# Kernel tuning notes

Measured on AMD Instinct MI355X. Metric: run time of the kernel, lower is better.

## Reference

```python
import jax, jax.numpy as jnp
import numpy as np

B, S, V, E, H, A, L = 64, 256, 32000, 512, 512, 512, 2
EPS = 1e-5


def _ln(x, g, b):
    m = jnp.mean(x, axis=-1, keepdims=True)
    v = jnp.mean((x - m) ** 2, axis=-1, keepdims=True)
    return (x - m) * jax.lax.rsqrt(v + EPS) * g + b


def _lstm_cell(x, h, c, W_ih, W_hh, b_ih, b_hh):
    # torch gate order: i, f, g, o
    gates = x @ W_ih.T + b_ih + h @ W_hh.T + b_hh  # [B, 4H]
    i, f, g, o = jnp.split(gates, 4, axis=-1)
    i, f, o = jax.nn.sigmoid(i), jax.nn.sigmoid(f), jax.nn.sigmoid(o)
    g = jnp.tanh(g)
    c_new = f * c + i * g
    h_new = o * jnp.tanh(c_new)
    return h_new, c_new


def setup_inputs() -> dict:
    key = jax.random.key(0)
    ks = jax.random.split(key, 24)
    d = {}
    d['input_token'] = jax.random.randint(ks[0], (B, 1), 0, V)
    d['h0'] = jax.random.normal(ks[1], (L, B, H), jnp.float32)
    d['c0'] = jax.random.normal(ks[2], (L, B, H), jnp.float32)
    d['encoder_outputs'] = jax.random.normal(ks[3], (B, S, 2 * H), jnp.float32)
    d['encoder_mask'] = jnp.ones((B, S), jnp.int32)
    sc = lambda fi, fo: float(np.sqrt(6.0 / (fi + fo)))
    d['emb'] = jax.random.normal(ks[4], (V, E), jnp.float32) * 0.1
    d['ln_emb_g'] = jnp.ones((E,), jnp.float32)
    d['ln_emb_b'] = jnp.zeros((E,), jnp.float32)
    d['W_enc'] = jax.random.uniform(ks[5], (A, 2 * H), jnp.float32, -sc(2 * H, A), sc(2 * H, A))
    d['b_enc'] = jnp.zeros((A,), jnp.float32)
    d['W_dec'] = jax.random.uniform(ks[6], (A, H), jnp.float32, -sc(H, A), sc(H, A))
    d['b_dec'] = jnp.zeros((A,), jnp.float32)
    d['v_att'] = jax.random.uniform(ks[7], (1, A), jnp.float32, -sc(A, 1), sc(A, 1))
    d['ln_att_g'] = jnp.ones((A,), jnp.float32)
    d['ln_att_b'] = jnp.zeros((A,), jnp.float32)
    in0, in1 = E + 2 * H, H
    d['W_ih0'] = jax.random.uniform(ks[8], (4 * H, in0), jnp.float32, -sc(in0, 4 * H), sc(in0, 4 * H))
    d['W_hh0'] = jax.random.normal(ks[9], (4 * H, H), jnp.float32) * 0.05
    d['b_ih0'] = jnp.zeros((4 * H,), jnp.float32).at[H:2 * H].set(1.0)
    d['b_hh0'] = jnp.zeros((4 * H,), jnp.float32)
    d['W_ih1'] = jax.random.uniform(ks[10], (4 * H, in1), jnp.float32, -sc(in1, 4 * H), sc(in1, 4 * H))
    d['W_hh1'] = jax.random.normal(ks[11], (4 * H, H), jnp.float32) * 0.05
    d['b_ih1'] = jnp.zeros((4 * H,), jnp.float32).at[H:2 * H].set(1.0)
    d['b_hh1'] = jnp.zeros((4 * H,), jnp.float32)
    d['ln_lstm_g'] = jnp.ones((H,), jnp.float32)
    d['ln_lstm_b'] = jnp.zeros((H,), jnp.float32)
    d['W_ctx'] = jax.random.uniform(ks[12], (H, 2 * H), jnp.float32, -sc(2 * H, H), sc(2 * H, H))
    d['b_ctx'] = jnp.zeros((H,), jnp.float32)
    d['W_out'] = jax.random.uniform(ks[13], (V, H), jnp.float32, -sc(H, V), sc(H, V))
    d['b_out'] = jnp.zeros((V,), jnp.float32)
    return d


def reference(input_token, h0, c0, encoder_outputs, encoder_mask,
              emb, ln_emb_g, ln_emb_b,
              W_enc, b_enc, W_dec, b_dec, v_att, ln_att_g, ln_att_b,
              W_ih0, W_hh0, b_ih0, b_hh0, W_ih1, W_hh1, b_ih1, b_hh1,
              ln_lstm_g, ln_lstm_b, W_ctx, b_ctx, W_out, b_out):
    # embedding + norm (dropout = identity in eval)
    embedded = _ln(emb[input_token], ln_emb_g, ln_emb_b)  # [B,1,E]

    # attention using top-layer hidden state
    dec_h = h0[-1]  # [B,H]
    enc_proj = jnp.einsum('bsk,ak->bsa', encoder_outputs, W_enc) + b_enc
    dec_proj = dec_h @ W_dec.T + b_dec  # [B,A]
    combined = _ln(enc_proj + dec_proj[:, None, :], ln_att_g, ln_att_b)
    scores = jnp.einsum('bsa,a->bs', jnp.tanh(combined), v_att[0])
    scores = jnp.where(encoder_mask == 0, -jnp.inf, scores)
    attn_w = jax.nn.softmax(scores, axis=1)  # [B,S]
    context = jnp.einsum('bs,bsk->bk', attn_w, encoder_outputs)  # [B,2H]

    # single-step 2-layer LSTM
    x = jnp.concatenate([embedded[:, 0, :], context], axis=-1)  # [B,E+2H]
    h_l0, c_l0 = _lstm_cell(x, h0[0], c0[0], W_ih0, W_hh0, b_ih0, b_hh0)
    h_l1, c_l1 = _lstm_cell(h_l0, h0[1], c0[1], W_ih1, W_hh1, b_ih1, b_hh1)
    h_new = jnp.stack([h_l0, h_l1])
    c_new = jnp.stack([c_l0, c_l1])

    lstm_out = _ln(h_l1, ln_lstm_g, ln_lstm_b)  # [B,H]
    proj_ctx = context @ W_ctx.T + b_ctx  # [B,H]
    logits = (lstm_out + proj_ctx) @ W_out.T + b_out  # [B,V]
    return logits[:, None, :], (h_new, c_new), attn_w
```

## Files before the change

kernel.cpp:

```cpp
#include <hip/hip_runtime.h>

typedef unsigned int u32;
typedef unsigned short u16;
typedef __attribute__((ext_vector_type(8))) short short8;
typedef __attribute__((ext_vector_type(4))) float f32x4;

__device__ __forceinline__ float bf2f(u16 u) {
  union { u32 i; float f; } v; v.i = ((u32)u) << 16; return v.f;
}
__device__ __forceinline__ u16 f2bf(float f) {
  union { float f; u32 i; } v; v.f = f;
  u32 u = v.i;
  u += 0x7FFFu + ((u >> 16) & 1u);
  return (u16)(u >> 16);
}
__device__ __forceinline__ float tanh_fast(float x) {
  float e = __expf(-2.f * fabsf(x));
  float r = (1.f - e) / (1.f + e);
  return x < 0.f ? -r : r;
}
__device__ __forceinline__ float sigmoid_fast(float x) {
  return 1.f / (1.f + __expf(-x));
}
template<bool F32>
__device__ __forceinline__ float ld1(const void* p, size_t i) {
  return F32 ? ((const float*)p)[i] : bf2f(((const u16*)p)[i]);
}
__device__ __forceinline__ void outst(void* p, size_t i, float v, int f32o) {
  if (f32o) ((float*)p)[i] = v; else ((u16*)p)[i] = f2bf(v);
}

#define GLL16(gp, lp) __builtin_amdgcn_global_load_lds( \
    (__attribute__((address_space(1))) void*)(gp), \
    (__attribute__((address_space(3))) void*)(lp), 16, 0, 0)

#define OFF_H    2048000
#define OFF_C    2113536
#define OFF_ATTN 2179072

#define A_LNAG 0
#define A_LNAB 512
#define A_VAT  1024
#define A_BENC 1536
#define A_BDEC 2048
#define A_BIH0 2560
#define A_BHH0 4608
#define A_BIH1 6656
#define A_BHH1 8704
#define A_LNLG 10752
#define A_LNLB 11264
#define A_BCTX 11776
#define A_BOUT 12288
#define A_TOTAL 44288

struct SrcPtrs {
  const void *h0, *c0, *emb, *lneg, *lneb, *Wenc, *benc, *Wdec, *bdec, *vat,
             *lnag, *lnab, *bih0, *bhh0, *bih1, *bhh1, *lnlg, *lnlb, *Wctx,
             *bctx, *bout;
  const int *tok;
};

__global__ void k_flag(const u32* __restrict__ lneg, int* __restrict__ flag) {
  if (threadIdx.x == 0) flag[0] = (lneg[0] == 0x3F800000u) ? 1 : 0;
}

template<bool F32>
__device__ __forceinline__ void convblk(const void* src, u16* dst, size_t base) {
  size_t i0 = base + (size_t)threadIdx.x * 16;
  if (F32) {
    const float* s = (const float*)src + i0;
    float4 a = *(const float4*)s, b = *(const float4*)(s + 4);
    float4 c = *(const float4*)(s + 8), d = *(const float4*)(s + 12);
    short8 v0, v1;
    v0[0]=(short)f2bf(a.x); v0[1]=(short)f2bf(a.y); v0[2]=(short)f2bf(a.z); v0[3]=(short)f2bf(a.w);
    v0[4]=(short)f2bf(b.x); v0[5]=(short)f2bf(b.y); v0[6]=(short)f2bf(b.z); v0[7]=(short)f2bf(b.w);
    v1[0]=(short)f2bf(c.x); v1[1]=(short)f2bf(c.y); v1[2]=(short)f2bf(c.z); v1[3]=(short)f2bf(c.w);
    v1[4]=(short)f2bf(d.x); v1[5]=(short)f2bf(d.y); v1[6]=(short)f2bf(d.z); v1[7]=(short)f2bf(d.w);
    *(short8*)(dst + i0) = v0; *(short8*)(dst + i0 + 8) = v1;
  } else {
    const uint4* s = (const uint4*)((const u16*)src + i0);
    uint4 a = s[0], b = s[1];
    *(uint4*)(dst + i0) = a; *((uint4*)(dst + i0) + 1) = b;
  }
}

template<bool F32>
__global__ __launch_bounds__(256) void k_conv(
    const int* __restrict__ flagp, SrcPtrs P,
    u16* __restrict__ xcat, u16* __restrict__ xcat1, u16* __restrict__ h1bf,
    float* __restrict__ c0f, float* __restrict__ arena,
    u16* __restrict__ Wencbf, u16* __restrict__ Wdecbf, u16* __restrict__ Wctxbf)
{
  if (flagp[0] != (F32 ? 1 : 0)) return;
  __shared__ float red[8];
  const int t = threadIdx.x;
  const int blk = blockIdx.x;
  if (blk < 64) {
    const int b = blk;
    const int tk = P.tok[b];
    float e0 = ld1<F32>(P.emb, (size_t)tk * 512 + t);
    float e1 = ld1<F32>(P.emb, (size_t)tk * 512 + t + 256);
    float s = e0 + e1, ss = e0 * e0 + e1 * e1;
    #pragma unroll
    for (int o = 1; o < 64; o <<= 1) { s += __shfl_xor(s, o, 64); ss += __shfl_xor(ss, o, 64); }
    if ((t & 63) == 0) { red[t >> 6] = s; red[4 + (t >> 6)] = ss; }
    __syncthreads();
    s = red[0] + red[1] + red[2] + red[3];
    ss = red[4] + red[5] + red[6] + red[7];
    const float mean = s * (1.f / 512.f);
    const float rstd = rsqrtf(fmaxf(ss * (1.f / 512.f) - mean * mean, 0.f) + 1e-5f);
    xcat[b*2048 + t]       = f2bf((e0 - mean) * rstd * ld1<F32>(P.lneg, t) + ld1<F32>(P.lneb, t));
    xcat[b*2048 + t + 256] = f2bf((e1 - mean) * rstd * ld1<F32>(P.lneg, t + 256) + ld1<F32>(P.lneb, t + 256));
    xcat[b*2048 + 1536 + t]       = f2bf(ld1<F32>(P.h0, (size_t)b * 512 + t));
    xcat[b*2048 + 1536 + t + 256] = f2bf(ld1<F32>(P.h0, (size_t)b * 512 + t + 256));
  } else if (blk < 128) {
    const int b = blk - 64;
    for (int j = t; j < 512; j += 256) {
      float h1 = ld1<F32>(P.h0, 32768 + (size_t)b * 512 + j);
      xcat1[b*1024 + 512 + j] = f2bf(h1);
      h1bf[b*512 + j] = f2bf(h1);
      c0f[b*512 + j]         = ld1<F32>(P.c0, (size_t)b * 512 + j);
      c0f[32768 + b*512 + j] = ld1<F32>(P.c0, 32768 + (size_t)b * 512 + j);
    }
  } else if (blk < 256) {
    const int qb = (blk - 128) * 512;
    #pragma unroll
    for (int u = 0; u < 2; u++) {
      int Qi = qb + u * 256 + t;
      int kc = Qi >> 11, rem = Qi & 2047;
      int cq = rem >> 9, col = rem & 511;
      size_t src = (size_t)col * 1024 + kc * 32 + cq * 8;
      if (F32) {
        const float* s = (const float*)P.Wenc + src;
        float4 a = *(const float4*)s, b2 = *(const float4*)(s + 4);
        short8 v;
        v[0]=(short)f2bf(a.x); v[1]=(short)f2bf(a.y); v[2]=(short)f2bf(a.z); v[3]=(short)f2bf(a.w);
        v[4]=(short)f2bf(b2.x); v[5]=(short)f2bf(b2.y); v[6]=(short)f2bf(b2.z); v[7]=(short)f2bf(b2.w);
        *(short8*)(Wencbf + (size_t)Qi * 8) = v;
      } else {
        *(uint4*)(Wencbf + (size_t)Qi * 8) = *(const uint4*)((const u16*)P.Wenc + src);
      }
    }
  } else if (blk < 320) {
    convblk<F32>(P.Wdec, Wdecbf, (size_t)(blk - 256) * 4096);
  } else if (blk < 448) {
    convblk<F32>(P.Wctx, Wctxbf, (size_t)(blk - 320) * 4096);
  } else {
    int base = (blk - 448) * 4096;
    for (int i = t; i < 4096; i += 256) {
      int v = base + i;
      if (v >= A_TOTAL) break;
      const void* s; int off;
      if      (v < 512)   { s = P.lnag; off = v; }
      else if (v < 1024)  { s = P.lnab; off = v - 512; }
      else if (v < 1536)  { s = P.vat;  off = v - 1024; }
      else if (v < 2048)  { s = P.benc; off = v - 1536; }
      else if (v < 2560)  { s = P.bdec; off = v - 2048; }
      else if (v < 4608)  { s = P.bih0; off = v - 2560; }
      else if (v < 6656)  { s = P.bhh0; off = v - 4608; }
      else if (v < 8704)  { s = P.bih1; off = v - 6656; }
      else if (v < 10752) { s = P.bhh1; off = v - 8704; }
      else if (v < 11264) { s = P.lnlg; off = v - 10752; }
      else if (v < 11776) { s = P.lnlb; off = v - 11264; }
      else if (v < 12288) { s = P.bctx; off = v - 11776; }
      else                { s = P.bout; off = v - 12288; }
      arena[v] = ld1<F32>(s, off);
    }
  }
}

__global__ __launch_bounds__(256) void k_dproj(
    const u16* __restrict__ h1bf, const u16* __restrict__ Wdecbf,
    const float* __restrict__ arena, float* __restrict__ dpf)
{
  __shared__ float hs[512];
  __shared__ float part[256];
  const int t = threadIdx.x;
  const int b = blockIdx.x >> 2, cg = blockIdx.x & 3;
  {
    u32 u2 = *(const u32*)(h1bf + b * 512 + t * 2);
    hs[t * 2]     = bf2f((u16)(u2 & 0xffff));
    hs[t * 2 + 1] = bf2f((u16)(u2 >> 16));
  }
  __syncthreads();
  const int col = cg * 128 + (t & 127);
  const int kh = (t >> 7) * 256;
  const u16* w = Wdecbf + (size_t)col * 512 + kh;
  float acc = 0.f;
  #pragma unroll 4
  for (int k = 0; k < 256; k += 8) {
    short8 wv = *(const short8*)(w + k);
    #pragma unroll
    for (int i = 0; i < 8; i++) acc += hs[kh + k + i] * bf2f((u16)wv[i]);
  }
  part[t] = acc;
  __syncthreads();
  if (t < 128) {
    float v = part[t] + part[t + 128];
    dpf[b * 512 + col] = v + arena[A_BENC + col] + arena[A_BDEC + col];
  }
}

__global__ __launch_bounds__(512, 2) void k_scores(
    const int* __restrict__ flagp,
    const void* __restrict__ enc, const u16* __restrict__ WencT,
    const float* __restrict__ dpf, const float* __restrict__ arena,
    const int* __restrict__ mask, float* __restrict__ scores)
{
  const int f32w = flagp[0];
  __shared__ __align__(16) char sm[73728];
  const int t = threadIdx.x, wave = t >> 6, lane = t & 63;
  const int q = lane >> 4, r15 = lane & 15;
  const int m0 = blockIdx.x * 64, b = m0 >> 8, n0 = wave * 64;
  const int arow = t >> 2, acq = t & 3;

  float4 rA0, rA1;

  auto stageB = [&](int buf, int kt) {
    char* Bb = sm + buf * 32768;
    #pragma unroll
    for (int r = 0; r < 4; ++r) {
      int chunk = (wave << 2) + r;
      const u16* g = WencT + (size_t)kt * 16384 + (size_t)(chunk * 64 + lane) * 8;
      GLL16(g, Bb + chunk * 1024);
    }
  };
  auto stageAb = [&](int buf, int kc) {
    if (wave < 4) {
      int row = lane ^ (wave << 1);
      const u16* g = (const u16*)enc + (size_t)(m0 + row) * 1024 + kc + (wave << 3);
      GLL16(g, sm + 65536 + buf * 4096 + (wave << 10));
    }
  };
  auto issueAf = [&](int kc) {
    const float* p = (const float*)enc + (size_t)(m0 + arow) * 1024 + kc + (acq << 3);
    rA0 = *(const float4*)p; rA1 = *(const float4*)(p + 4);
  };
  auto writeAf = [&](int buf) {
    short8 v;
    v[0]=(short)f2bf(rA0.x); v[1]=(short)f2bf(rA0.y); v[2]=(short)f2bf(rA0.z); v[3]=(short)f2bf(rA0.w);
    v[4]=(short)f2bf(rA1.x); v[5]=(short)f2bf(rA1.y); v[6]=(short)f2bf(rA1.z); v[7]=(short)f2bf(rA1.w);
    int slot = (acq << 6) + (arow ^ (acq << 1));
    *(short8*)(sm + 65536 + buf * 4096 + slot * 16) = v;
  };

  if (f32w) { if (t < 256) issueAf(0); }
  stageB(0, 0);
  if (!f32w) stageAb(0, 0);
  if (f32w && t < 256) writeAf(0);
  __syncthreads();

  f32x4 acc[4][4] = {};
  int cur = 0;
  for (int kt = 0; kt < 32; ++kt) {
    const int more = (kt + 1 < 32);
    if (more) {
      if (f32w) { if (t < 256) issueAf((kt + 1) << 5); }
      stageB(cur ^ 1, kt + 1);
      if (!f32w) stageAb(cur ^ 1, (kt + 1) << 5);
    }
    const char* Ab = sm + 65536 + cur * 4096;
    const char* Bb = sm + cur * 32768;
    short8 af[4], bfr[4];
    #pragma unroll
    for (int mi = 0; mi < 4; mi++) {
      int slot = (q << 6) + ((mi * 16 + r15) ^ (q << 1));
      af[mi] = *(const short8*)(Ab + slot * 16);
    }
    #pragma unroll
    for (int ni = 0; ni < 4; ni++)
      bfr[ni] = *(const short8*)(Bb + ((q << 9) + n0 + ni * 16 + r15) * 16);
    #pragma unroll
    for (int mi = 0; mi < 4; mi++)
      #pragma unroll
      for (int ni = 0; ni < 4; ni++)
        acc[mi][ni] = __builtin_amdgcn_mfma_f32_16x16x32_bf16(af[mi], bfr[ni], acc[mi][ni], 0, 0, 0);
    if (more && f32w && t < 256) writeAf(cur ^ 1);
    __syncthreads();
    cur ^= 1;
  }

  float dpv[4];
  #pragma unroll
  for (int ni = 0; ni < 4; ni++)
    dpv[ni] = dpf[b * 512 + n0 + ni * 16 + r15];

  float* ps    = (float*)sm;
  float* pq    = (float*)(sm + 2048);
  float* mean_ = (float*)(sm + 4096);
  float* rstd_ = (float*)(sm + 4352);
  #pragma unroll
  for (int mi = 0; mi < 4; mi++)
    #pragma unroll
    for (int r = 0; r < 4; r++) {
      float s = 0.f, sq = 0.f;
      #pragma unroll
      for (int ni = 0; ni < 4; ni++) {
        float x = acc[mi][ni][r] + dpv[ni];
        s += x; sq += x * x;
      }
      #pragma unroll
      for (int o = 1; o < 16; o <<= 1) { s += __shfl_xor(s, o, 64); sq += __shfl_xor(sq, o, 64); }
      if (r15 == 0) { int row = mi*16 + q*4 + r; ps[wave*64 + row] = s; pq[wave*64 + row] = sq; }
    }
  __syncthreads();
  if (t < 64) {
    float s = 0.f, sq = 0.f;
    #pragma unroll
    for (int w = 0; w < 8; w++) { s += ps[w*64 + t]; sq += pq[w*64 + t]; }
    float mn = s * (1.f / 512.f);
    mean_[t] = mn;
    rstd_[t] = rsqrtf(fmaxf(sq * (1.f / 512.f) - mn * mn, 0.f) + 1e-5f);
  }
  __syncthreads();
  float g4[4], b4[4], v4[4];
  #pragma unroll
  for (int ni = 0; ni < 4; ni++) {
    int col = n0 + ni*16 + r15;
    g4[ni] = arena[A_LNAG + col]; b4[ni] = arena[A_LNAB + col]; v4[ni] = arena[A_VAT + col];
  }
  #pragma unroll
  for (int mi = 0; mi < 4; mi++)
    #pragma unroll
    for (int r = 0; r < 4; r++) {
      int row = mi*16 + q*4 + r;
      float mn = mean_[row], rs = rstd_[row];
      float s = 0.f;
      #pragma unroll
      for (int ni = 0; ni < 4; ni++) {
        float x = acc[mi][ni][r] + dpv[ni];
        float y = (x - mn) * rs * g4[ni] + b4[ni];
        s += tanh_fast(y) * v4[ni];
      }
      #pragma unroll
      for (int o = 1; o < 16; o <<= 1) s += __shfl_xor(s, o, 64);
      if (r15 == 0) ps[wave*64 + row] = s;
    }
  __syncthreads();
  if (t < 64) {
    float sc = 0.f;
    #pragma unroll
    for (int w = 0; w < 8; w++) sc += ps[w*64 + t];
    int s_ = (m0 & 255) + t;
    scores[m0 + t] = mask[b*256 + s_] ? sc : -__builtin_inff();
  }
}

__global__ __launch_bounds__(256) void k_softmax_ctx(
    const int* __restrict__ flagp,
    const float* __restrict__ scores, const void* __restrict__ enc,
    u16* __restrict__ xcat, void* __restrict__ out)
{
  const int f32w = flagp[0];
  __shared__ float aw[256];
  __shared__ float red[8];
  __shared__ float px[512];
  const int t = threadIdx.x;
  const int b = blockIdx.x >> 2, kq = blockIdx.x & 3;
  float sv = scores[b * 256 + t];
  float mx = sv;
  #pragma unroll
  for (int o = 1; o < 64; o <<= 1) mx = fmaxf(mx, __shfl_xor(mx, o, 64));
  if ((t & 63) == 0) red[t >> 6] = mx;
  __syncthreads();
  mx = fmaxf(fmaxf(red[0], red[1]), fmaxf(red[2], red[3]));
  float e = __expf(sv - mx);
  float s = e;
  #pragma unroll
  for (int o = 1; o < 64; o <<= 1) s += __shfl_xor(s, o, 64);
  if ((t & 63) == 0) red[4 + (t >> 6)] = s;
  __syncthreads();
  s = red[4] + red[5] + red[6] + red[7];
  float w = e / s;
  aw[t] = w;
  if (kq == 0) outst(out, OFF_ATTN + b * 256 + t, w, f32w);
  __syncthreads();
  const int kk = t & 127, sg = t >> 7;
  float a0 = 0.f, a1 = 0.f;
  if (f32w) {
    const float* p = (const float*)enc + (size_t)b * 262144 + kq * 256 + kk * 2;
    #pragma unroll 4
    for (int i = 0; i < 128; i++) {
      int si = i * 2 + sg;
      float2 v = *(const float2*)(p + (size_t)si * 1024);
      a0 += aw[si] * v.x; a1 += aw[si] * v.y;
    }
  } else {
    const u16* p = (const u16*)enc + (size_t)b * 262144 + kq * 256 + kk * 2;
    #pragma unroll 4
    for (int i = 0; i < 128; i++) {
      int si = i * 2 + sg;
      u32 u = *(const u32*)(p + (size_t)si * 1024);
      a0 += aw[si] * bf2f((u16)(u & 0xffff)); a1 += aw[si] * bf2f((u16)(u >> 16));
    }
  }
  px[sg * 256 + kk * 2]     = a0;
  px[sg * 256 + kk * 2 + 1] = a1;
  __syncthreads();
  float cv = px[t] + px[256 + t];
  xcat[b * 2048 + 512 + kq * 256 + t] = f2bf(cv);
}

__global__ __launch_bounds__(512) void k_lstm(
    const int* __restrict__ flagp,
    const u16* __restrict__ x, int K,
    const void* __restrict__ Wa, int Ka,
    const void* __restrict__ Wb, int Kb,
    int boff_ih, int boff_hh,
    const float* __restrict__ arena, const float* __restrict__ c0f, int coff,
    void* __restrict__ out, size_t h_off, size_t c_off,
    u16* __restrict__ aux_bf, float* __restrict__ aux_f)
{
  const int f32w = flagp[0];
  __shared__ __align__(16) char sm[40960];
  const int t = threadIdx.x, wave = t >> 6, lane = t & 63;
  const int q = lane >> 4, r15 = lane & 15;
  const int jt = blockIdx.x;
  const int kslice = K >> 3, ksteps = kslice >> 5;
  const int k0 = wave * kslice;
  const void* W; int Kw, koff;
  if (k0 < Ka) { W = Wa; Kw = Ka; koff = k0; }
  else         { W = Wb; Kw = Kb; koff = k0 - Ka; }
  char* slab = sm + wave * 5120;
  const int bc = lane >> 2, bcq = lane & 3;
  const int wrow = (bc >> 2) * 512 + jt * 4 + (bc & 3);
  f32x4 acc4[4] = {};

  for (int st = 0; st < ksteps; ++st) {
    const int kA = k0 + st * 32;
    const int kB = koff + st * 32;
    #pragma unroll
    for (int i = 0; i < 4; i++) {
      int id = i * 64 + lane;
      int row = id >> 2, cq = id & 3;
      *(uint4*)(slab + (cq * 64 + row) * 16) = *(const uint4*)(x + (size_t)row * K + kA + cq * 8);
    }
    {
      size_t wi = (size_t)wrow * Kw + kB + bcq * 8;
      short8 bv;
      if (f32w) {
        const float* wp = (const float*)W + wi;
        float4 a = *(const float4*)wp, b = *(const float4*)(wp + 4);
        bv[0]=(short)f2bf(a.x); bv[1]=(short)f2bf(a.y); bv[2]=(short)f2bf(a.z); bv[3]=(short)f2bf(a.w);
        bv[4]=(short)f2bf(b.x); bv[5]=(short)f2bf(b.y); bv[6]=(short)f2bf(b.z); bv[7]=(short)f2bf(b.w);
      } else {
        bv = *(const short8*)((const u16*)W + wi);
      }
      *(short8*)(slab + 4096 + (bcq * 16 + bc) * 16) = bv;
    }
    short8 af[4];
    #pragma unroll
    for (int mi = 0; mi < 4; mi++)
      af[mi] = *(const short8*)(slab + (q * 64 + mi * 16 + r15) * 16);
    short8 bfrg = *(const short8*)(slab + 4096 + (q * 16 + r15) * 16);
    #pragma unroll
    for (int mi = 0; mi < 4; mi++)
      acc4[mi] = __builtin_amdgcn_mfma_f32_16x16x32_bf16(af[mi], bfrg, acc4[mi], 0, 0, 0);
  }
  __syncthreads();
  float* part = (float*)sm;
  #pragma unroll
  for (int mi = 0; mi < 4; mi++)
    #pragma unroll
    for (int r = 0; r < 4; r++)
      part[wave * 1024 + (mi * 16 + q * 4 + r) * 16 + r15] = acc4[mi][r];
  __syncthreads();
  if (t < 256) {
    const int b_ = t >> 2, cl = t & 3;
    const int jg = jt * 4 + cl;
    float g4[4];
    #pragma unroll
    for (int g = 0; g < 4; g++) {
      float v = 0.f;
      #pragma unroll
      for (int w = 0; w < 8; w++) v += part[w * 1024 + b_ * 16 + g * 4 + cl];
      g4[g] = v + arena[boff_ih + g * 512 + jg] + arena[boff_hh + g * 512 + jg];
    }
    float i_ = sigmoid_fast(g4[0]), f_ = sigmoid_fast(g4[1]), o_ = sigmoid_fast(g4[3]);
    float gg = tanh_fast(g4[2]);
    float c_ = f_ * c0f[coff + b_ * 512 + jg] + i_ * gg;
    float h_ = o_ * tanh_fast(c_);
    outst(out, h_off + b_ * 512 + jg, h_, f32w);
    outst(out, c_off + b_ * 512 + jg, c_, f32w);
    if (aux_bf) aux_bf[b_ * 1024 + jg] = f2bf(h_);
    if (aux_f)  aux_f[b_ * 512 + jg] = h_;
  }
}

__global__ __launch_bounds__(256) void k_svec(
    const float* __restrict__ hl1f, const u16* __restrict__ xcat,
    const u16* __restrict__ Wctxbf, const float* __restrict__ arena,
    u16* __restrict__ svec)
{
  __shared__ float ctx[1024];
  __shared__ float red[8];
  const int t = threadIdx.x, b = blockIdx.x;
  for (int i = t; i < 1024; i += 256) ctx[i] = bf2f(xcat[b * 2048 + 512 + i]);
  float h0v = hl1f[b * 512 + t], h1v = hl1f[b * 512 + t + 256];
  float s = h0v + h1v, ss = h0v * h0v + h1v * h1v;
  #pragma unroll
  for (int o = 1; o < 64; o <<= 1) { s += __shfl_xor(s, o, 64); ss += __shfl_xor(ss, o, 64); }
  if ((t & 63) == 0) { red[t >> 6] = s; red[4 + (t >> 6)] = ss; }
  __syncthreads();
  s = red[0] + red[1] + red[2] + red[3];
  ss = red[4] + red[5] + red[6] + red[7];
  const float mean = s * (1.f / 512.f);
  const float rstd = rsqrtf(fmaxf(ss * (1.f / 512.f) - mean * mean, 0.f) + 1e-5f);
  for (int hh = t; hh < 512; hh += 256) {
    float hv = hl1f[b * 512 + hh];
    float lnv = (hv - mean) * rstd * arena[A_LNLG + hh] + arena[A_LNLB + hh];
    float acc = arena[A_BCTX + hh];
    #pragma unroll 4
    for (int k = 0; k < 1024; k += 8) {
      short8 wv = *(const short8*)(Wctxbf + (size_t)hh * 1024 + k);
      #pragma unroll
      for (int i = 0; i < 8; i++) acc += ctx[k + i] * bf2f((u16)wv[i]);
    }
    svec[b * 512 + hh] = f2bf(lnv + acc);
  }
}

__global__ __launch_bounds__(256) void k_logits(
    const int* __restrict__ flagp,
    const u16* __restrict__ svec, const void* __restrict__ Wout,
    const float* __restrict__ arena, void* __restrict__ out)
{
  const int f32w = flagp[0];
  __shared__ __align__(16) char sm[8192];
  const int t = threadIdx.x, wave = t >> 6, lane = t & 63;
  const int q = lane >> 4, r15 = lane & 15;
  const int nb = blockIdx.x * 128;
  float4 ra[2], rb[2]; uint4 rc[2];
  auto issue = [&](int kc) {
    #pragma unroll
    for (int i = 0; i < 2; i++) {
      int c = i * 256 + t;
      int row = c >> 2, cq = c & 3;
      size_t off = (size_t)(nb + row) * 512 + kc * 32 + cq * 8;
      if (f32w) {
        const float* p = (const float*)Wout + off;
        ra[i] = *(const float4*)p; rb[i] = *(const float4*)(p + 4);
      } else {
        rc[i] = *(const uint4*)((const u16*)Wout + off);
      }
    }
  };
  issue(0);
  f32x4 acc[4][2] = {};
  for (int kc = 0; kc < 16; kc++) {
    #pragma unroll
    for (int i = 0; i < 2; i++) {
      int c = i * 256 + t;
      int row = c >> 2, cq = c & 3;
      if (f32w) {
        short8 v;
        v[0]=(short)f2bf(ra[i].x); v[1]=(short)f2bf(ra[i].y); v[2]=(short)f2bf(ra[i].z); v[3]=(short)f2bf(ra[i].w);
        v[4]=(short)f2bf(rb[i].x); v[5]=(short)f2bf(rb[i].y); v[6]=(short)f2bf(rb[i].z); v[7]=(short)f2bf(rb[i].w);
        *(short8*)(sm + (cq * 128 + row) * 16) = v;
      } else {
        *(uint4*)(sm + (cq * 128 + row) * 16) = rc[i];
      }
    }
    __syncthreads();
    if (kc + 1 < 16) issue(kc + 1);
    short8 af[4], bfr[2];
    #pragma unroll
    for (int mi = 0; mi < 4; mi++)
      af[mi] = *(const short8*)(svec + (size_t)(mi * 16 + r15) * 512 + kc * 32 + q * 8);
    #pragma unroll
    for (int ni = 0; ni < 2; ni++)
      bfr[ni] = *(const short8*)(sm + (q * 128 + wave * 32 + ni * 16 + r15) * 16);
    #pragma unroll
    for (int mi = 0; mi < 4; mi++)
      #pragma unroll
      for (int ni = 0; ni < 2; ni++)
        acc[mi][ni] = __builtin_amdgcn_mfma_f32_16x16x32_bf16(af[mi], bfr[ni], acc[mi][ni], 0, 0, 0);
    __syncthreads();
  }
  #pragma unroll
  for (int ni = 0; ni < 2; ni++) {
    int col = nb + wave * 32 + ni * 16 + r15;
    float bo = arena[A_BOUT + col];
    #pragma unroll
    for (int mi = 0; mi < 4; mi++)
      #pragma unroll
      for (int r = 0; r < 4; r++) {
        int brow = mi * 16 + q * 4 + r;
        outst(out, (size_t)brow * 32000 + col, acc[mi][ni][r] + bo, f32w);
      }
  }
}

extern "C" void kernel_launch(void* const* d_in, const int* in_sizes, int n_in,
                              void* d_out, int out_size, void* d_ws, size_t ws_size,
                              hipStream_t stream)
{
  SrcPtrs P;
  P.tok  = (const int*)d_in[0];
  P.h0   = d_in[1];  P.c0   = d_in[2];
  const void* enc = d_in[3];
  const int* mask = (const int*)d_in[4];
  P.emb  = d_in[5]; P.lneg = d_in[6]; P.lneb = d_in[7];
  P.Wenc = d_in[8]; P.benc = d_in[9]; P.Wdec = d_in[10]; P.bdec = d_in[11];
  P.vat  = d_in[12]; P.lnag = d_in[13]; P.lnab = d_in[14];
  P.bih0 = d_in[17]; P.bhh0 = d_in[18];
  P.bih1 = d_in[21]; P.bhh1 = d_in[22];
  P.lnlg = d_in[23]; P.lnlb = d_in[24];
  P.Wctx = d_in[25]; P.bctx = d_in[26];
  const void* Wout = d_in[27];
  P.bout = d_in[28];
  const void* Wih0 = d_in[15];
  const void* Whh0 = d_in[16];
  const void* Wih1 = d_in[19];
  const void* Whh1 = d_in[20];

  char* ws = (char*)d_ws;
  int*   flag    = (int*)(ws + 0);
  float* arena   = (float*)(ws + 256);
  u16*   Wencbf  = (u16*)(ws + 177664);
  u16*   Wdecbf  = (u16*)(ws + 1226240);
  u16*   Wctxbf  = (u16*)(ws + 1750528);
  u16*   xcat    = (u16*)(ws + 2799104);
  u16*   xcat1   = (u16*)(ws + 3061248);
  u16*   h1bf    = (u16*)(ws + 3192320);
  float* c0f     = (float*)(ws + 3257856);
  float* scores  = (float*)(ws + 3520000);
  float* hl1f    = (float*)(ws + 3585536);
  u16*   svec    = (u16*)(ws + 3716608);
  float* dpf     = (float*)(ws + 3782144);

  k_flag<<<1, 64, 0, stream>>>((const u32*)P.lneg, flag);
  k_conv<false><<<460, 256, 0, stream>>>(flag, P, xcat, xcat1, h1bf, c0f, arena, Wencbf, Wdecbf, Wctxbf);
  k_conv<true ><<<460, 256, 0, stream>>>(flag, P, xcat, xcat1, h1bf, c0f, arena, Wencbf, Wdecbf, Wctxbf);
  k_dproj<<<256, 256, 0, stream>>>(h1bf, Wdecbf, arena, dpf);
  k_scores<<<256, 512, 0, stream>>>(flag, enc, Wencbf, dpf, arena, mask, scores);
  k_softmax_ctx<<<256, 256, 0, stream>>>(flag, scores, enc, xcat, d_out);
  k_lstm<<<128, 512, 0, stream>>>(flag, xcat, 2048, Wih0, 1536, Whh0, 512,
                                  A_BIH0, A_BHH0, arena, c0f, 0,
                                  d_out, OFF_H, OFF_C, xcat1, (float*)nullptr);
  k_lstm<<<128, 512, 0, stream>>>(flag, xcat1, 1024, Wih1, 512, Whh1, 512,
                                  A_BIH1, A_BHH1, arena, c0f, 32768,
                                  d_out, OFF_H + 32768, OFF_C + 32768,
                                  (u16*)nullptr, hl1f);
  k_svec<<<64, 256, 0, stream>>>(hl1f, xcat, Wctxbf, arena, svec);
  k_logits<<<250, 256, 0, stream>>>(flag, svec, Wout, arena, d_out);
}
```

Baseline: 388.2 us.

## Halve M-tile in scores and N-tile in logits, widen context loads, double-buffer logits

The scores kernel now processes 32 encoder rows per block instead of 64 and launches 512 blocks, with the A-tile staging and the LN reductions resized to match. The logits kernel uses 64 output columns per block across 500 blocks and gains a double-buffered LDS pipeline, so the next K-chunk's global loads overlap the MFMAs. The softmax-context kernel reads four values per thread with float4 loads over four s-groups. The aim is more blocks across the many CUs and better latency hiding in the memory-bound stages. The cost is less reuse of the staged W_enc tile per block, since each block still loads the full B operand for only half as many rows.

```diff
diff --git a/kernel.cpp b/kernel.cpp
--- a/kernel.cpp
+++ b/kernel.cpp
@@ -201,17 +201,17 @@
   }
 }
 
-__global__ __launch_bounds__(512, 2) void k_scores(
+__global__ __launch_bounds__(512, 4) void k_scores(
     const int* __restrict__ flagp,
     const void* __restrict__ enc, const u16* __restrict__ WencT,
     const float* __restrict__ dpf, const float* __restrict__ arena,
     const int* __restrict__ mask, float* __restrict__ scores)
 {
   const int f32w = flagp[0];
-  __shared__ __align__(16) char sm[73728];
+  __shared__ __align__(16) char sm[69632];
   const int t = threadIdx.x, wave = t >> 6, lane = t & 63;
   const int q = lane >> 4, r15 = lane & 15;
-  const int m0 = blockIdx.x * 64, b = m0 >> 8, n0 = wave * 64;
+  const int m0 = blockIdx.x * 32, b = m0 >> 8, n0 = wave * 64;
   const int arow = t >> 2, acq = t & 3;
 
   float4 rA0, rA1;
@@ -226,10 +226,12 @@
     }
   };
   auto stageAb = [&](int buf, int kc) {
-    if (wave < 4) {
-      int row = lane ^ (wave << 1);
-      const u16* g = (const u16*)enc + (size_t)(m0 + row) * 1024 + kc + (wave << 3);
-      GLL16(g, sm + 65536 + buf * 4096 + (wave << 10));
+    if (wave < 2) {
+      int s = (wave << 6) + lane;
+      int cq = s >> 5, rowslot = s & 31;
+      int row = rowslot ^ (cq << 1);
+      const u16* g = (const u16*)enc + (size_t)(m0 + row) * 1024 + kc + (cq << 3);
+      GLL16(g, sm + 65536 + buf * 2048 + (wave << 10));
     }
   };
   auto issueAf = [&](int kc) {
@@ -240,42 +242,42 @@
     short8 v;
     v[0]=(short)f2bf(rA0.x); v[1]=(short)f2bf(rA0.y); v[2]=(short)f2bf(rA0.z); v[3]=(short)f2bf(rA0.w);
     v[4]=(short)f2bf(rA1.x); v[5]=(short)f2bf(rA1.y); v[6]=(short)f2bf(rA1.z); v[7]=(short)f2bf(rA1.w);
-    int slot = (acq << 6) + (arow ^ (acq << 1));
-    *(short8*)(sm + 65536 + buf * 4096 + slot * 16) = v;
+    int slot = (acq << 5) + (arow ^ (acq << 1));
+    *(short8*)(sm + 65536 + buf * 2048 + slot * 16) = v;
   };
 
-  if (f32w) { if (t < 256) issueAf(0); }
+  if (f32w) { if (t < 128) issueAf(0); }
   stageB(0, 0);
   if (!f32w) stageAb(0, 0);
-  if (f32w && t < 256) writeAf(0);
-  __syncthreads();
-
-  f32x4 acc[4][4] = {};
+  if (f32w && t < 128) writeAf(0);
+  __syncthreads();
+
+  f32x4 acc[2][4] = {};
   int cur = 0;
   for (int kt = 0; kt < 32; ++kt) {
     const int more = (kt + 1 < 32);
     if (more) {
-      if (f32w) { if (t < 256) issueAf((kt + 1) << 5); }
+      if (f32w) { if (t < 128) issueAf((kt + 1) << 5); }
       stageB(cur ^ 1, kt + 1);
       if (!f32w) stageAb(cur ^ 1, (kt + 1) << 5);
     }
-    const char* Ab = sm + 65536 + cur * 4096;
+    const char* Ab = sm + 65536 + cur * 2048;
     const char* Bb = sm + cur * 32768;
-    short8 af[4], bfr[4];
-    #pragma unroll
-    for (int mi = 0; mi < 4; mi++) {
-      int slot = (q << 6) + ((mi * 16 + r15) ^ (q << 1));
+    short8 af[2], bfr[4];
+    #pragma unroll
+    for (int mi = 0; mi < 2; mi++) {
+      int slot = (q << 5) + ((mi * 16 + r15) ^ (q << 1));
       af[mi] = *(const short8*)(Ab + slot * 16);
     }
     #pragma unroll
     for (int ni = 0; ni < 4; ni++)
       bfr[ni] = *(const short8*)(Bb + ((q << 9) + n0 + ni * 16 + r15) * 16);
     #pragma unroll
-    for (int mi = 0; mi < 4; mi++)
+    for (int mi = 0; mi < 2; mi++)
       #pragma unroll
       for (int ni = 0; ni < 4; ni++)
         acc[mi][ni] = __builtin_amdgcn_mfma_f32_16x16x32_bf16(af[mi], bfr[ni], acc[mi][ni], 0, 0, 0);
-    if (more && f32w && t < 256) writeAf(cur ^ 1);
+    if (more && f32w && t < 128) writeAf(cur ^ 1);
     __syncthreads();
     cur ^= 1;
   }
@@ -286,11 +288,11 @@
     dpv[ni] = dpf[b * 512 + n0 + ni * 16 + r15];
 
   float* ps    = (float*)sm;
-  float* pq    = (float*)(sm + 2048);
-  float* mean_ = (float*)(sm + 4096);
-  float* rstd_ = (float*)(sm + 4352);
-  #pragma unroll
-  for (int mi = 0; mi < 4; mi++)
+  float* pq    = (float*)(sm + 1024);
+  float* mean_ = (float*)(sm + 2048);
+  float* rstd_ = (float*)(sm + 2176);
+  #pragma unroll
+  for (int mi = 0; mi < 2; mi++)
     #pragma unroll
     for (int r = 0; r < 4; r++) {
       float s = 0.f, sq = 0.f;
@@ -301,13 +303,13 @@
       }
       #pragma unroll
       for (int o = 1; o < 16; o <<= 1) { s += __shfl_xor(s, o, 64); sq += __shfl_xor(sq, o, 64); }
-      if (r15 == 0) { int row = mi*16 + q*4 + r; ps[wave*64 + row] = s; pq[wave*64 + row] = sq; }
-    }
-  __syncthreads();
-  if (t < 64) {
+      if (r15 == 0) { int row = mi*16 + q*4 + r; ps[wave*32 + row] = s; pq[wave*32 + row] = sq; }
+    }
+  __syncthreads();
+  if (t < 32) {
     float s = 0.f, sq = 0.f;
     #pragma unroll
-    for (int w = 0; w < 8; w++) { s += ps[w*64 + t]; sq += pq[w*64 + t]; }
+    for (int w = 0; w < 8; w++) { s += ps[w*32 + t]; sq += pq[w*32 + t]; }
     float mn = s * (1.f / 512.f);
     mean_[t] = mn;
     rstd_[t] = rsqrtf(fmaxf(sq * (1.f / 512.f) - mn * mn, 0.f) + 1e-5f);
@@ -320,7 +322,7 @@
     g4[ni] = arena[A_LNAG + col]; b4[ni] = arena[A_LNAB + col]; v4[ni] = arena[A_VAT + col];
   }
   #pragma unroll
-  for (int mi = 0; mi < 4; mi++)
+  for (int mi = 0; mi < 2; mi++)
     #pragma unroll
     for (int r = 0; r < 4; r++) {
       int row = mi*16 + q*4 + r;
@@ -334,13 +336,13 @@
       }
       #pragma unroll
       for (int o = 1; o < 16; o <<= 1) s += __shfl_xor(s, o, 64);
-      if (r15 == 0) ps[wave*64 + row] = s;
-    }
-  __syncthreads();
-  if (t < 64) {
+      if (r15 == 0) ps[wave*32 + row] = s;
+    }
+  __syncthreads();
+  if (t < 32) {
     float sc = 0.f;
     #pragma unroll
-    for (int w = 0; w < 8; w++) sc += ps[w*64 + t];
+    for (int w = 0; w < 8; w++) sc += ps[w*32 + t];
     int s_ = (m0 & 255) + t;
     scores[m0 + t] = mask[b*256 + s_] ? sc : -__builtin_inff();
   }
@@ -354,7 +356,7 @@
   const int f32w = flagp[0];
   __shared__ float aw[256];
   __shared__ float red[8];
-  __shared__ float px[512];
+  __shared__ float px[1024];
   const int t = threadIdx.x;
   const int b = blockIdx.x >> 2, kq = blockIdx.x & 3;
   float sv = scores[b * 256 + t];
@@ -375,29 +377,34 @@
   aw[t] = w;
   if (kq == 0) outst(out, OFF_ATTN + b * 256 + t, w, f32w);
   __syncthreads();
-  const int kk = t & 127, sg = t >> 7;
-  float a0 = 0.f, a1 = 0.f;
+  const int kk = t & 63, sg = t >> 6;
+  float a0 = 0.f, a1 = 0.f, a2 = 0.f, a3 = 0.f;
   if (f32w) {
-    const float* p = (const float*)enc + (size_t)b * 262144 + kq * 256 + kk * 2;
-    #pragma unroll 4
-    for (int i = 0; i < 128; i++) {
-      int si = i * 2 + sg;
-      float2 v = *(const float2*)(p + (size_t)si * 1024);
-      a0 += aw[si] * v.x; a1 += aw[si] * v.y;
+    const float* p = (const float*)enc + (size_t)b * 262144 + kq * 256 + kk * 4;
+    #pragma unroll 8
+    for (int i = 0; i < 64; i++) {
+      int si = i * 4 + sg;
+      float4 v = *(const float4*)(p + (size_t)si * 1024);
+      float w_ = aw[si];
+      a0 += w_ * v.x; a1 += w_ * v.y; a2 += w_ * v.z; a3 += w_ * v.w;
     }
   } else {
-    const u16* p = (const u16*)enc + (size_t)b * 262144 + kq * 256 + kk * 2;
-    #pragma unroll 4
-    for (int i = 0; i < 128; i++) {
-      int si = i * 2 + sg;
-      u32 u = *(const u32*)(p + (size_t)si * 1024);
-      a0 += aw[si] * bf2f((u16)(u & 0xffff)); a1 += aw[si] * bf2f((u16)(u >> 16));
-    }
-  }
-  px[sg * 256 + kk * 2]     = a0;
-  px[sg * 256 + kk * 2 + 1] = a1;
-  __syncthreads();
-  float cv = px[t] + px[256 + t];
+    const u16* p = (const u16*)enc + (size_t)b * 262144 + kq * 256 + kk * 4;
+    #pragma unroll 8
+    for (int i = 0; i < 64; i++) {
+      int si = i * 4 + sg;
+      uint2 u = *(const uint2*)(p + (size_t)si * 1024);
+      float w_ = aw[si];
+      a0 += w_ * bf2f((u16)(u.x & 0xffff)); a1 += w_ * bf2f((u16)(u.x >> 16));
+      a2 += w_ * bf2f((u16)(u.y & 0xffff)); a3 += w_ * bf2f((u16)(u.y >> 16));
+    }
+  }
+  px[sg * 256 + kk * 4]     = a0;
+  px[sg * 256 + kk * 4 + 1] = a1;
+  px[sg * 256 + kk * 4 + 2] = a2;
+  px[sg * 256 + kk * 4 + 3] = a3;
+  __syncthreads();
+  float cv = px[t] + px[256 + t] + px[512 + t] + px[768 + t];
   xcat[b * 2048 + 512 + kq * 256 + t] = f2bf(cv);
 }
 
@@ -529,64 +536,62 @@
   __shared__ __align__(16) char sm[8192];
   const int t = threadIdx.x, wave = t >> 6, lane = t & 63;
   const int q = lane >> 4, r15 = lane & 15;
-  const int nb = blockIdx.x * 128;
-  float4 ra[2], rb[2]; uint4 rc[2];
+  const int nb = blockIdx.x * 64;
+  const int row = t >> 2, cq = t & 3;
+  float4 ra, rb; uint4 rc;
   auto issue = [&](int kc) {
-    #pragma unroll
-    for (int i = 0; i < 2; i++) {
-      int c = i * 256 + t;
-      int row = c >> 2, cq = c & 3;
-      size_t off = (size_t)(nb + row) * 512 + kc * 32 + cq * 8;
-      if (f32w) {
-        const float* p = (const float*)Wout + off;
-        ra[i] = *(const float4*)p; rb[i] = *(const float4*)(p + 4);
-      } else {
-        rc[i] = *(const uint4*)((const u16*)Wout + off);
-      }
+    size_t off = (size_t)(nb + row) * 512 + kc * 32 + cq * 8;
+    if (f32w) {
+      const float* p = (const float*)Wout + off;
+      ra = *(const float4*)p; rb = *(const float4*)(p + 4);
+    } else {
+      rc = *(const uint4*)((const u16*)Wout + off);
+    }
+  };
+  auto wr = [&](int buf) {
+    int slot = (cq << 6) + (row ^ (cq << 1));
+    if (f32w) {
+      short8 v;
+      v[0]=(short)f2bf(ra.x); v[1]=(short)f2bf(ra.y); v[2]=(short)f2bf(ra.z); v[3]=(short)f2bf(ra.w);
+      v[4]=(short)f2bf(rb.x); v[5]=(short)f2bf(rb.y); v[6]=(short)f2bf(rb.z); v[7]=(short)f2bf(rb.w);
+      *(short8*)(sm + buf * 4096 + slot * 16) = v;
+    } else {
+      *(uint4*)(sm + buf * 4096 + slot * 16) = rc;
     }
   };
   issue(0);
-  f32x4 acc[4][2] = {};
+  wr(0);
+  __syncthreads();
+  f32x4 acc[4] = {};
+  int cur = 0;
   for (int kc = 0; kc < 16; kc++) {
-    #pragma unroll
-    for (int i = 0; i < 2; i++) {
-      int c = i * 256 + t;
-      int row = c >> 2, cq = c & 3;
-      if (f32w) {
-        short8 v;
-        v[0]=(short)f2bf(ra[i].x); v[1]=(short)f2bf(ra[i].y); v[2]=(short)f2bf(ra[i].z); v[3]=(short)f2bf(ra[i].w);
-        v[4]=(short)f2bf(rb[i].x); v[5]=(short)f2bf(rb[i].y); v[6]=(short)f2bf(rb[i].z); v[7]=(short)f2bf(rb[i].w);
-        *(short8*)(sm + (cq * 128 + row) * 16) = v;
-      } else {
-        *(uint4*)(sm + (cq * 128 + row) * 16) = rc[i];
-      }
-    }
-    __syncthreads();
-    if (kc + 1 < 16) issue(kc + 1);
-    short8 af[4], bfr[2];
+    const int more = (kc + 1 < 16);
+    if (more) issue(kc + 1);
+    short8 af[4], bfr;
     #pragma unroll
     for (int mi = 0; mi < 4; mi++)
       af[mi] = *(const short8*)(svec + (size_t)(mi * 16 + r15) * 512 + kc * 32 + q * 8);
-    #pragma unroll
-    for (int ni = 0; ni < 2; ni++)
-      bfr[ni] = *(const short8*)(sm + (q * 128 + wave * 32 + ni * 16 + r15) * 16);
+    {
+      int col = wave * 16 + r15;
+      int slot = (q << 6) + (col ^ (q << 1));
+      bfr = *(const short8*)(sm + cur * 4096 + slot * 16);
+    }
     #pragma unroll
     for (int mi = 0; mi < 4; mi++)
-      #pragma unroll
-      for (int ni = 0; ni < 2; ni++)
-        acc[mi][ni] = __builtin_amdgcn_mfma_f32_16x16x32_bf16(af[mi], bfr[ni], acc[mi][ni], 0, 0, 0);
+      acc[mi] = __builtin_amdgcn_mfma_f32_16x16x32_bf16(af[mi], bfr, acc[mi], 0, 0, 0);
+    if (more) wr(cur ^ 1);
     __syncthreads();
-  }
-  #pragma unroll
-  for (int ni = 0; ni < 2; ni++) {
-    int col = nb + wave * 32 + ni * 16 + r15;
+    cur ^= 1;
+  }
+  {
+    int col = nb + wave * 16 + r15;
     float bo = arena[A_BOUT + col];
     #pragma unroll
     for (int mi = 0; mi < 4; mi++)
       #pragma unroll
       for (int r = 0; r < 4; r++) {
         int brow = mi * 16 + q * 4 + r;
-        outst(out, (size_t)brow * 32000 + col, acc[mi][ni][r] + bo, f32w);
+        outst(out, (size_t)brow * 32000 + col, acc[mi][r] + bo, f32w);
       }
   }
 }
@@ -633,7 +638,7 @@
   k_conv<false><<<460, 256, 0, stream>>>(flag, P, xcat, xcat1, h1bf, c0f, arena, Wencbf, Wdecbf, Wctxbf);
   k_conv<true ><<<460, 256, 0, stream>>>(flag, P, xcat, xcat1, h1bf, c0f, arena, Wencbf, Wdecbf, Wctxbf);
   k_dproj<<<256, 256, 0, stream>>>(h1bf, Wdecbf, arena, dpf);
-  k_scores<<<256, 512, 0, stream>>>(flag, enc, Wencbf, dpf, arena, mask, scores);
+  k_scores<<<512, 512, 0, stream>>>(flag, enc, Wencbf, dpf, arena, mask, scores);
   k_softmax_ctx<<<256, 256, 0, stream>>>(flag, scores, enc, xcat, d_out);
   k_lstm<<<128, 512, 0, stream>>>(flag, xcat, 2048, Wih0, 1536, Whh0, 512,
                                   A_BIH0, A_BHH0, arena, c0f, 0,
@@ -643,5 +648,5 @@
                                   d_out, OFF_H + 32768, OFF_C + 32768,
                                   (u16*)nullptr, hl1f);
   k_svec<<<64, 256, 0, stream>>>(hl1f, xcat, Wctxbf, arena, svec);
-  k_logits<<<250, 256, 0, stream>>>(flag, svec, Wout, arena, d_out);
-}
+  k_logits<<<500, 256, 0, stream>>>(flag, svec, Wout, arena, d_out);
+}
```

Result: no change. 390.8 us (+0.7%).
